# Kernel tuning notes

Hardware: AMD Instinct MI355X
Metric: run time of the kernel (lower is better)

The kernel has to match this reference:

```python
import math
import jax, jax.numpy as jnp
import numpy as np

N_HEAD = 16
HEAD_DIM = 128


def _rope(x, cos, sin):
    # x: (B,T,H,D); cos,sin: (T,1,D/2) broadcast over B,H
    d = x.shape[-1] // 2
    x1, x2 = x[..., :d], x[..., d:]
    return jnp.concatenate([x1 * cos + x2 * sin, -x1 * sin + x2 * cos], axis=-1)


def _rms_norm(x, eps=1e-6):
    return x * jax.lax.rsqrt(jnp.mean(x * x, axis=-1, keepdims=True) + eps)


def setup_inputs() -> dict:
    key = jax.random.key(0)
    ks = jax.random.split(key, 9)
    B, T, C = 2, 2048, 2048
    scale = 1.0 / math.sqrt(C)
    return {
        "x": jax.random.normal(ks[0], (B, T, C), jnp.float32),
        "ve": jax.random.normal(ks[1], (B, T, C), jnp.float32),
        "Wq": jax.random.normal(ks[2], (C, C), jnp.float32) * scale,
        "Wk": jax.random.normal(ks[3], (C, C), jnp.float32) * scale,
        "Wv": jax.random.normal(ks[4], (C, C), jnp.float32) * scale,
        "Wproj": jax.random.normal(ks[5], (C, C), jnp.float32) * scale,
        "Wgate": jax.random.normal(ks[6], (N_HEAD, 12), jnp.float32) * (1.0 / math.sqrt(12.0)),
        "cos": jax.random.uniform(ks[7], (T, 1, HEAD_DIM // 2), jnp.float32),
        "sin": jax.random.uniform(ks[8], (T, 1, HEAD_DIM // 2), jnp.float32),
        "window_left": 1024,
    }


def reference(x, ve, Wq, Wk, Wv, Wproj, Wgate, cos, sin, window_left):
    B, T, C = x.shape
    H, D = N_HEAD, HEAD_DIM

    # Linear projections (torch Linear: x @ W.T)
    q = (x @ Wq.T).reshape(B, T, H, D)
    k = (x @ Wk.T).reshape(B, T, H, D)
    v = (x @ Wv.T).reshape(B, T, H, D)

    # value-embedding gating (has_ve layer)
    gate = 3.0 * jax.nn.sigmoid(x[..., :12] @ Wgate.T)  # (B,T,H)
    v = v + gate[..., None] * ve.reshape(B, T, H, D)

    # rope + qk rms-norm * 1.2
    q = _rms_norm(_rope(q, cos, sin)) * 1.2
    k = _rms_norm(_rope(k, cos, sin)) * 1.2

    # windowed causal mask
    row = jnp.arange(T)[:, None]
    col = jnp.arange(T)[None, :]
    mask = row >= col
    if 0 < window_left < T:
        mask = mask & (row - col <= window_left)
    bias = jnp.where(mask, 0.0, -1e9).astype(x.dtype)  # (T,T)

    scale = 1.0 / math.sqrt(D)
    att = jnp.einsum("bqhd,bkhd->bhqk", q, k) * scale + bias[None, None]
    att = jax.nn.softmax(att, axis=-1)
    y = jnp.einsum("bhqk,bkhd->bqhd", att, v).reshape(B, T, H * D)
    return y @ Wproj.T
```

## Files before the change

### kernel.cpp

```cpp
#include <hip/hip_runtime.h>
#include <hip/hip_bf16.h>
#include <cstdint>

#define N_HEAD 16
#define HEAD_DIM 128

typedef __bf16 bf16;
typedef __bf16 bf16x8 __attribute__((ext_vector_type(8)));
typedef __bf16 bf16x4 __attribute__((ext_vector_type(4)));
typedef float f32x4 __attribute__((ext_vector_type(4)));

__device__ __forceinline__ void gload_lds16(const void* g, void* l) {
  auto gp = reinterpret_cast<const __attribute__((address_space(1))) char*>(
      reinterpret_cast<uintptr_t>(g));
  auto lp = reinterpret_cast<__attribute__((address_space(3))) char*>(
      reinterpret_cast<uintptr_t>(l));
  __builtin_amdgcn_global_load_lds(gp, lp, 16, 0, 0);
}

__global__ __launch_bounds__(256) void cvt_all(
    const float* __restrict__ x, const float* __restrict__ Wq,
    const float* __restrict__ Wk, const float* __restrict__ Wv,
    const float* __restrict__ Wp, bf16* __restrict__ xb,
    bf16* __restrict__ wqkv, bf16* __restrict__ wpb, int nx4, int nw4) {
  const int z = blockIdx.z;
  const float* in;
  bf16* out;
  int n4;
  if (z == 0)      { in = x;  out = xb;  n4 = nx4; }
  else if (z == 1) { in = Wq; out = wqkv;                     n4 = nw4; }
  else if (z == 2) { in = Wk; out = wqkv + (size_t)nw4 * 4;   n4 = nw4; }
  else if (z == 3) { in = Wv; out = wqkv + (size_t)nw4 * 8;   n4 = nw4; }
  else             { in = Wp; out = wpb;  n4 = nw4; }
  const int i = blockIdx.x * 256 + threadIdx.x;
  if (i >= n4) return;
  const float4 f = reinterpret_cast<const float4*>(in)[i];
  bf16x4 o;
  o.x = (bf16)f.x; o.y = (bf16)f.y; o.z = (bf16)f.z; o.w = (bf16)f.w;
  reinterpret_cast<bf16x4*>(out)[i] = o;
}

template <typename OutT>
__global__ __launch_bounds__(256) void gemm_bt(
    const bf16* __restrict__ A, const bf16* __restrict__ Bt,
    OutT* __restrict__ C, int M, int N, int K) {
  __shared__ __align__(16) bf16 As[128 * 32];
  __shared__ __align__(16) bf16 Bs[128 * 32];
  const int tid = threadIdx.x;
  const int lane = tid & 63;
  const int wave = tid >> 6;
  const int wm = (wave >> 1) * 64;
  const int wn = (wave & 1) * 64;
  const int lr = lane & 15;
  const int lk = (lane >> 4) * 8;

  const bf16* Ab = A + (size_t)blockIdx.y * 128 * K;
  const bf16* Bb = Bt + (size_t)blockIdx.x * 128 * K;

  const int r0 = tid >> 2;
  const int c0 = (tid & 3) * 8;

  f32x4 acc[4][4] = {};

  for (int k0 = 0; k0 < K; k0 += 32) {
    __syncthreads();
    gload_lds16(Ab + (size_t)r0 * K + k0 + c0, As + (size_t)tid * 8);
    gload_lds16(Ab + (size_t)(r0 + 64) * K + k0 + c0, As + (size_t)(256 + tid) * 8);
    gload_lds16(Bb + (size_t)r0 * K + k0 + c0, Bs + (size_t)tid * 8);
    gload_lds16(Bb + (size_t)(r0 + 64) * K + k0 + c0, Bs + (size_t)(256 + tid) * 8);
    __syncthreads();

    bf16x8 a[4], b[4];
#pragma unroll
    for (int i = 0; i < 4; ++i)
      a[i] = *reinterpret_cast<const bf16x8*>(As + (wm + i * 16 + lr) * 32 + lk);
#pragma unroll
    for (int j = 0; j < 4; ++j)
      b[j] = *reinterpret_cast<const bf16x8*>(Bs + (wn + j * 16 + lr) * 32 + lk);
#pragma unroll
    for (int i = 0; i < 4; ++i)
#pragma unroll
      for (int j = 0; j < 4; ++j)
        acc[i][j] = __builtin_amdgcn_mfma_f32_16x16x32_bf16(a[i], b[j], acc[i][j], 0, 0, 0);
  }

  const int orow = blockIdx.y * 128 + wm + (lane >> 4) * 4;
  const int ocol = blockIdx.x * 128 + wn + lr;
#pragma unroll
  for (int i = 0; i < 4; ++i)
#pragma unroll
    for (int j = 0; j < 4; ++j)
#pragma unroll
      for (int r = 0; r < 4; ++r)
        C[(size_t)(orow + i * 16 + r) * N + (ocol + j * 16)] = (OutT)acc[i][j][r];
}

__global__ __launch_bounds__(256) void rope_rms(
    bf16* __restrict__ qkv, const float* __restrict__ cs,
    const float* __restrict__ sn, int T) {
  const int C = N_HEAD * HEAD_DIM;
  const int S = 3 * C;
  const int bt = blockIdx.x;
  const int t = bt % T;
  const int wave = threadIdx.x >> 6;
  const int lane = threadIdx.x & 63;
  const int h = blockIdx.y * 4 + wave;
  bf16* p = qkv + (size_t)bt * S + (blockIdx.z ? C : 0) + h * HEAD_DIM;
  const float oscale = blockIdx.z ? 1.2f : 0.15302091809294977f;
  const float c = cs[t * 64 + lane];
  const float s = sn[t * 64 + lane];
  const float x1 = (float)p[lane];
  const float x2 = (float)p[lane + 64];
  const float r1 = x1 * c + x2 * s;
  const float r2 = x2 * c - x1 * s;
  float ss = r1 * r1 + r2 * r2;
#pragma unroll
  for (int m = 1; m < 64; m <<= 1) ss += __shfl_xor(ss, m);
  const float sc = oscale * rsqrtf(ss * (1.0f / 128.0f) + 1e-6f);
  p[lane] = (bf16)(r1 * sc);
  p[lane + 64] = (bf16)(r2 * sc);
}

__global__ __launch_bounds__(256) void gate_transpose(
    const bf16* __restrict__ qkv, const float* __restrict__ x,
    const float* __restrict__ ve, const float* __restrict__ Wg,
    bf16* __restrict__ vT, int T) {
  const int C = N_HEAD * HEAD_DIM;
  const int S = 3 * C;
  const int t0 = blockIdx.x * 64;
  const int c0 = blockIdx.y * 64;
  const int b = blockIdx.z;
  const int h = c0 >> 7;

  __shared__ float gs[64];
  __shared__ __align__(16) bf16 tile[64][72];

  if (threadIdx.x < 64) {
    const float* xr = x + (size_t)(b * T + t0 + threadIdx.x) * C;
    float a = 0.f;
#pragma unroll
    for (int j = 0; j < 12; ++j) a += xr[j] * Wg[h * 12 + j];
    gs[threadIdx.x] = 3.f / (1.f + __expf(-a));
  }
  __syncthreads();

  {
    const int r = threadIdx.x >> 2;
    const int cc = (threadIdx.x & 3) * 16;
    const size_t vrow = (size_t)(b * T + t0 + r) * S + 2 * C + c0 + cc;
    const size_t erow = (size_t)(b * T + t0 + r) * C + c0 + cc;
    bf16x8 a0 = *reinterpret_cast<const bf16x8*>(qkv + vrow);
    bf16x8 a1 = *reinterpret_cast<const bf16x8*>(qkv + vrow + 8);
    const float g = gs[r];
    bf16x8 o0, o1;
#pragma unroll
    for (int i = 0; i < 8; ++i) o0[i] = (bf16)((float)a0[i] + g * ve[erow + i]);
#pragma unroll
    for (int i = 0; i < 8; ++i) o1[i] = (bf16)((float)a1[i] + g * ve[erow + 8 + i]);
    *reinterpret_cast<bf16x8*>(&tile[r][cc]) = o0;
    *reinterpret_cast<bf16x8*>(&tile[r][cc + 8]) = o1;
  }
  __syncthreads();
  {
    const int dr = threadIdx.x >> 2;
    const int tc = (threadIdx.x & 3) * 16;
    bf16x8 o0, o1;
#pragma unroll
    for (int i = 0; i < 8; ++i) o0[i] = tile[tc + i][dr];
#pragma unroll
    for (int i = 0; i < 8; ++i) o1[i] = tile[tc + 8 + i][dr];
    const size_t orow =
        ((size_t)((b * N_HEAD + h) * HEAD_DIM) + (c0 & 127) + dr) * T + t0 + tc;
    *reinterpret_cast<bf16x8*>(vT + orow) = o0;
    *reinterpret_cast<bf16x8*>(vT + orow + 8) = o1;
  }
}

__global__ __launch_bounds__(256, 2) void attn(
    const bf16* __restrict__ qkv, const bf16* __restrict__ vT,
    bf16* __restrict__ y, const int* __restrict__ wptr, int T) {
  const int C = N_HEAD * HEAD_DIM;
  const int S = 3 * C;
  const int qb = blockIdx.x * 128;
  const int h = blockIdx.y;
  const int b = blockIdx.z;
  const int tid = threadIdx.x;
  const int wave = tid >> 6;
  const int lane = tid & 63;
  const int lm = lane & 15;
  const int quad = lane >> 4;

  const int w = wptr[0];
  const int W = (w > 0 && w < T) ? w : (1 << 30);

  __shared__ __align__(16) bf16 Ks[4][64][32];
  __shared__ __align__(16) bf16 Vs[2][128][32];
  __shared__ __align__(16) bf16 Pb[4][16][72];

  const bf16* kb = qkv + (size_t)b * T * S + C + (size_t)h * HEAD_DIM;
  const bf16* vb = vT + (size_t)((b * N_HEAD + h) * HEAD_DIM) * T;

  const int qt[2] = {qb + wave * 16, qb + 64 + wave * 16};
  bf16x8 qf[2][4];
#pragma unroll
  for (int t = 0; t < 2; ++t) {
    const bf16* qrow = qkv + (size_t)(b * T + qt[t] + lm) * S + h * HEAD_DIM;
#pragma unroll
    for (int c = 0; c < 4; ++c)
      qf[t][c] = *reinterpret_cast<const bf16x8*>(qrow + c * 32 + quad * 8);
  }

  float mrun[2] = {-1e30f, -1e30f}, lrun[2] = {0.f, 0.f};
  f32x4 oacc[2][8] = {};

  int kstart = qb - W;
  if (kstart < 0) kstart = 0;
  kstart &= ~63;

  const int sr = tid >> 2;
  const int sc = (tid & 3) * 8;

  for (int kc = kstart; kc <= qb + 127; kc += 64) {
    __syncthreads();
#pragma unroll
    for (int c = 0; c < 4; ++c)
      gload_lds16(kb + (size_t)(kc + sr) * S + c * 32 + sc, &Ks[c][0][0] + tid * 8);
#pragma unroll
    for (int c2 = 0; c2 < 2; ++c2)
#pragma unroll
      for (int i = 0; i < 2; ++i)
        gload_lds16(vb + (size_t)(i * 64 + sr) * T + kc + c2 * 32 + sc,
                    &Vs[c2][i * 64][0] + tid * 8);
    __syncthreads();

#pragma unroll
    for (int t = 0; t < 2; ++t) {
      const int q0 = qt[t];
      if (kc > q0 + 15 || kc + 63 < q0 - W) continue;
      const int qr = q0 + lm;

      f32x4 st[4] = {};
#pragma unroll
      for (int g = 0; g < 4; ++g)
#pragma unroll
        for (int c = 0; c < 4; ++c) {
          const bf16x8 kf =
              *reinterpret_cast<const bf16x8*>(&Ks[c][g * 16 + lm][quad * 8]);
          st[g] = __builtin_amdgcn_mfma_f32_16x16x32_bf16(kf, qf[t][c], st[g], 0, 0, 0);
        }
      float mx = -1e30f;
#pragma unroll
      for (int g = 0; g < 4; ++g)
#pragma unroll
        for (int r = 0; r < 4; ++r) {
          const int key = kc + g * 16 + quad * 4 + r;
          const bool valid = (key <= qr) && (qr - key <= W);
          st[g][r] = valid ? st[g][r] : -1e30f;
          mx = fmaxf(mx, st[g][r]);
        }
      mx = fmaxf(mx, __shfl_xor(mx, 16));
      mx = fmaxf(mx, __shfl_xor(mx, 32));
      const float mnew = fmaxf(mrun[t], mx);
      const float alpha = __builtin_amdgcn_exp2f(mrun[t] - mnew);
      mrun[t] = mnew;
      float rs = 0.f;
#pragma unroll
      for (int g = 0; g < 4; ++g) {
        bf16x4 pk;
#pragma unroll
        for (int r = 0; r < 4; ++r) {
          const float p = __builtin_amdgcn_exp2f(st[g][r] - mnew);
          rs += p;
          pk[r] = (bf16)p;
        }
        *reinterpret_cast<bf16x4*>(&Pb[wave][lm][g * 16 + quad * 4]) = pk;
      }
      rs += __shfl_xor(rs, 16);
      rs += __shfl_xor(rs, 32);
      lrun[t] = lrun[t] * alpha + rs;
#pragma unroll
      for (int dc = 0; dc < 8; ++dc)
#pragma unroll
        for (int r = 0; r < 4; ++r) oacc[t][dc][r] *= alpha;
#pragma unroll
      for (int c2 = 0; c2 < 2; ++c2) {
        const bf16x8 pf =
            *reinterpret_cast<const bf16x8*>(&Pb[wave][lm][c2 * 32 + quad * 8]);
#pragma unroll
        for (int dc = 0; dc < 8; ++dc) {
          const bf16x8 vf =
              *reinterpret_cast<const bf16x8*>(&Vs[c2][dc * 16 + lm][quad * 8]);
          oacc[t][dc] = __builtin_amdgcn_mfma_f32_16x16x32_bf16(vf, pf, oacc[t][dc], 0, 0, 0);
        }
      }
    }
  }

#pragma unroll
  for (int t = 0; t < 2; ++t) {
    const float inv = 1.f / lrun[t];
    bf16* yr = y + (size_t)(b * T + qt[t] + lm) * C + h * HEAD_DIM;
#pragma unroll
    for (int dc = 0; dc < 8; ++dc) {
      bf16x4 o;
#pragma unroll
      for (int r = 0; r < 4; ++r) o[r] = (bf16)(oacc[t][dc][r] * inv);
      *reinterpret_cast<bf16x4*>(yr + dc * 16 + quad * 4) = o;
    }
  }
}

extern "C" void kernel_launch(void* const* d_in, const int* in_sizes, int n_in,
                              void* d_out, int out_size, void* d_ws, size_t ws_size,
                              hipStream_t stream) {
  const float* x  = (const float*)d_in[0];
  const float* ve = (const float*)d_in[1];
  const float* Wq = (const float*)d_in[2];
  const float* Wk = (const float*)d_in[3];
  const float* Wv = (const float*)d_in[4];
  const float* Wp = (const float*)d_in[5];
  const float* Wg = (const float*)d_in[6];
  const float* cs = (const float*)d_in[7];
  const float* sn = (const float*)d_in[8];
  const int*   wl = (const int*)d_in[9];
  float* out = (float*)d_out;

  const int C = N_HEAD * HEAD_DIM;
  const int T = in_sizes[7] / (HEAD_DIM / 2);
  const int B = in_sizes[0] / (T * C);
  const int M = B * T;

  bf16* xb   = (bf16*)d_ws;
  bf16* wqkv = xb   + (size_t)M * C;
  bf16* wpb  = wqkv + (size_t)3 * C * C;
  bf16* qkv  = wpb  + (size_t)C * C;
  bf16* ybuf = qkv  + (size_t)3 * M * C;
  bf16* vTb  = xb;

  const int nx4 = M * C / 4, nw4 = C * C / 4;
  cvt_all<<<dim3((nx4 + 255) / 256, 1, 5), 256, 0, stream>>>(
      x, Wq, Wk, Wv, Wp, xb, wqkv, wpb, nx4, nw4);

  gemm_bt<bf16><<<dim3(3 * C / 128, M / 128), 256, 0, stream>>>(xb, wqkv, qkv, M, 3 * C, C);

  rope_rms<<<dim3(M, N_HEAD / 4, 2), 256, 0, stream>>>(qkv, cs, sn, T);
  gate_transpose<<<dim3(T / 64, C / 64, B), 256, 0, stream>>>(qkv, x, ve, Wg, vTb, T);
  attn<<<dim3(T / 128, N_HEAD, B), 256, 0, stream>>>(qkv, vTb, ybuf, wl, T);

  gemm_bt<float><<<dim3(C / 128, M / 128), 256, 0, stream>>>(ybuf, wpb, out, M, C, C);
}
```

Baseline: 448.4 us.

## Deepen GEMM K-step, register-prefetch attention K/V, remap attention blocks per XCD

Result: faster. 426.1 us (-5.0%).

```diff
diff --git a/kernel.cpp b/kernel.cpp
--- a/kernel.cpp
+++ b/kernel.cpp
@@ -44,8 +44,8 @@
 __global__ __launch_bounds__(256) void gemm_bt(
     const bf16* __restrict__ A, const bf16* __restrict__ Bt,
     OutT* __restrict__ C, int M, int N, int K) {
-  __shared__ __align__(16) bf16 As[128 * 32];
-  __shared__ __align__(16) bf16 Bs[128 * 32];
+  __shared__ __align__(16) bf16 As[2][128 * 32];
+  __shared__ __align__(16) bf16 Bs[2][128 * 32];
   const int tid = threadIdx.x;
   const int lane = tid & 63;
   const int wave = tid >> 6;
@@ -62,26 +62,33 @@
 
   f32x4 acc[4][4] = {};
 
-  for (int k0 = 0; k0 < K; k0 += 32) {
+  for (int k0 = 0; k0 < K; k0 += 64) {
     __syncthreads();
-    gload_lds16(Ab + (size_t)r0 * K + k0 + c0, As + (size_t)tid * 8);
-    gload_lds16(Ab + (size_t)(r0 + 64) * K + k0 + c0, As + (size_t)(256 + tid) * 8);
-    gload_lds16(Bb + (size_t)r0 * K + k0 + c0, Bs + (size_t)tid * 8);
-    gload_lds16(Bb + (size_t)(r0 + 64) * K + k0 + c0, Bs + (size_t)(256 + tid) * 8);
+#pragma unroll
+    for (int s = 0; s < 2; ++s) {
+      const int kk = k0 + s * 32 + c0;
+      gload_lds16(Ab + (size_t)r0 * K + kk, As[s] + (size_t)tid * 8);
+      gload_lds16(Ab + (size_t)(r0 + 64) * K + kk, As[s] + (size_t)(256 + tid) * 8);
+      gload_lds16(Bb + (size_t)r0 * K + kk, Bs[s] + (size_t)tid * 8);
+      gload_lds16(Bb + (size_t)(r0 + 64) * K + kk, Bs[s] + (size_t)(256 + tid) * 8);
+    }
     __syncthreads();
 
-    bf16x8 a[4], b[4];
-#pragma unroll
-    for (int i = 0; i < 4; ++i)
-      a[i] = *reinterpret_cast<const bf16x8*>(As + (wm + i * 16 + lr) * 32 + lk);
-#pragma unroll
-    for (int j = 0; j < 4; ++j)
-      b[j] = *reinterpret_cast<const bf16x8*>(Bs + (wn + j * 16 + lr) * 32 + lk);
-#pragma unroll
-    for (int i = 0; i < 4; ++i)
+#pragma unroll
+    for (int s = 0; s < 2; ++s) {
+      bf16x8 a[4], b[4];
+#pragma unroll
+      for (int i = 0; i < 4; ++i)
+        a[i] = *reinterpret_cast<const bf16x8*>(As[s] + (wm + i * 16 + lr) * 32 + lk);
 #pragma unroll
       for (int j = 0; j < 4; ++j)
-        acc[i][j] = __builtin_amdgcn_mfma_f32_16x16x32_bf16(a[i], b[j], acc[i][j], 0, 0, 0);
+        b[j] = *reinterpret_cast<const bf16x8*>(Bs[s] + (wn + j * 16 + lr) * 32 + lk);
+#pragma unroll
+      for (int i = 0; i < 4; ++i)
+#pragma unroll
+        for (int j = 0; j < 4; ++j)
+          acc[i][j] = __builtin_amdgcn_mfma_f32_16x16x32_bf16(a[i], b[j], acc[i][j], 0, 0, 0);
+    }
   }
 
   const int orow = blockIdx.y * 128 + wm + (lane >> 4) * 4;
@@ -178,12 +185,20 @@
 
 __global__ __launch_bounds__(256, 2) void attn(
     const bf16* __restrict__ qkv, const bf16* __restrict__ vT,
-    bf16* __restrict__ y, const int* __restrict__ wptr, int T) {
+    bf16* __restrict__ y, const int* __restrict__ wptr, int T, int B) {
   const int C = N_HEAD * HEAD_DIM;
   const int S = 3 * C;
-  const int qb = blockIdx.x * 128;
-  const int h = blockIdx.y;
-  const int b = blockIdx.z;
+  const int nq = T >> 7;
+  const int ppx = (B * N_HEAD) >> 3;
+  const int bid = blockIdx.x;
+  const int xcd = bid & 7;
+  const int sl = bid >> 3;
+  const int pair = xcd * ppx + sl / nq;
+  const int qi = sl % nq;
+  const int b = pair / N_HEAD;
+  const int h = pair % N_HEAD;
+  const int qb = qi * 128;
+
   const int tid = threadIdx.x;
   const int wave = tid >> 6;
   const int lane = tid & 63;
@@ -216,22 +231,50 @@
   int kstart = qb - W;
   if (kstart < 0) kstart = 0;
   kstart &= ~63;
+  const int kend = qb + 64;
 
   const int sr = tid >> 2;
   const int sc = (tid & 3) * 8;
 
-  for (int kc = kstart; kc <= qb + 127; kc += 64) {
+  bf16x8 kpre[4], vpre[4];
+  {
+    const bf16* kr = kb + (size_t)(kstart + sr) * S + sc;
+#pragma unroll
+    for (int c = 0; c < 4; ++c)
+      kpre[c] = *reinterpret_cast<const bf16x8*>(kr + c * 32);
+#pragma unroll
+    for (int c2 = 0; c2 < 2; ++c2)
+#pragma unroll
+      for (int i = 0; i < 2; ++i)
+        vpre[c2 * 2 + i] = *reinterpret_cast<const bf16x8*>(
+            vb + (size_t)(i * 64 + sr) * T + kstart + c2 * 32 + sc);
+  }
+
+  for (int kc = kstart; kc <= kend; kc += 64) {
     __syncthreads();
 #pragma unroll
     for (int c = 0; c < 4; ++c)
-      gload_lds16(kb + (size_t)(kc + sr) * S + c * 32 + sc, &Ks[c][0][0] + tid * 8);
+      *reinterpret_cast<bf16x8*>(&Ks[c][sr][sc]) = kpre[c];
 #pragma unroll
     for (int c2 = 0; c2 < 2; ++c2)
 #pragma unroll
       for (int i = 0; i < 2; ++i)
-        gload_lds16(vb + (size_t)(i * 64 + sr) * T + kc + c2 * 32 + sc,
-                    &Vs[c2][i * 64][0] + tid * 8);
+        *reinterpret_cast<bf16x8*>(&Vs[c2][i * 64 + sr][sc]) = vpre[c2 * 2 + i];
     __syncthreads();
+
+    if (kc + 64 <= kend) {
+      const int kc2 = kc + 64;
+      const bf16* kr = kb + (size_t)(kc2 + sr) * S + sc;
+#pragma unroll
+      for (int c = 0; c < 4; ++c)
+        kpre[c] = *reinterpret_cast<const bf16x8*>(kr + c * 32);
+#pragma unroll
+      for (int c2 = 0; c2 < 2; ++c2)
+#pragma unroll
+        for (int i = 0; i < 2; ++i)
+          vpre[c2 * 2 + i] = *reinterpret_cast<const bf16x8*>(
+              vb + (size_t)(i * 64 + sr) * T + kc2 + c2 * 32 + sc);
+    }
 
 #pragma unroll
     for (int t = 0; t < 2; ++t) {
@@ -345,7 +388,7 @@
 
   rope_rms<<<dim3(M, N_HEAD / 4, 2), 256, 0, stream>>>(qkv, cs, sn, T);
   gate_transpose<<<dim3(T / 64, C / 64, B), 256, 0, stream>>>(qkv, x, ve, Wg, vTb, T);
-  attn<<<dim3(T / 128, N_HEAD, B), 256, 0, stream>>>(qkv, vTb, ybuf, wl, T);
+  attn<<<dim3(B * N_HEAD * (T / 128)), 256, 0, stream>>>(qkv, vTb, ybuf, wl, T, B);
 
   gemm_bt<float><<<dim3(C / 128, M / 128), 256, 0, stream>>>(ybuf, wpb, out, M, C, C);
 }
```
